# Optimization experiments

Measured on AMD Instinct MI355X. Metric: run time of the kernel, lower is better.

## Reference

```python
import jax, jax.numpy as jnp
import numpy as np

B, C, L, D, E, K = 64, 23, 26000, 64, 512, 3  # batch, chromosomes, bins/chr, d_model, eos_dim, num_states
V = C * L


def setup_inputs() -> dict:
    key = jax.random.key(0)
    k0, k1, k2, k3 = jax.random.split(key, 4)
    return {
        "eos_emb": jax.random.normal(k0, (B, C, E), jnp.float32),
        "bin_ids": jnp.arange(C * L, dtype=jnp.int32).reshape(C, L),
        "emb_table": jax.random.normal(k1, (V, D), jnp.float32) * 0.02,
        "eos_W": jax.random.normal(k2, (D, E), jnp.float32) / np.float32(np.sqrt(E)),
        "eos_b": jnp.zeros((D,), jnp.float32),
        "fc_W": jax.random.normal(k3, (K, 2 * D), jnp.float32) / np.float32(np.sqrt(2 * D)),
        "fc_b": jnp.zeros((K,), jnp.float32),
    }


def reference(eos_emb, bin_ids, emb_table, eos_W, eos_b, fc_W, fc_b):
    # eos_projection (use_eos_proj=True): [B,C,E] @ [D,E]^T + b -> [B,C,D]
    eos = jnp.einsum('bce,de->bcd', eos_emb, eos_W) + eos_b
    # per-chromosome embedding gather (bin_projection skipped: bin_emb_dim == d_model, use_bin_proj=False)
    bin_emb = emb_table[bin_ids]  # [C,L,D]
    # fc on concat([bin, eos]) == bin @ Wb^T + eos @ We^T + b (avoids materializing [B,C,L,2D])
    Wb, We = fc_W[:, :D], fc_W[:, D:]
    a = jnp.einsum('cld,kd->clk', bin_emb, Wb)          # [C,L,K]
    e = jnp.einsum('bcd,kd->bck', eos, We) + fc_b       # [B,C,K]
    return jax.nn.relu(a[None, :, :, :] + e[:, :, None, :])  # [B,C,L,K]
```

## Files before the change

kernel.cpp:

```cpp
#include <hip/hip_runtime.h>

#define NB 64
#define NC 23
#define NL 26000
#define ND 64
#define NE 512
#define NK 3
#define NCL (NC * NL)
#define FP4 (NL * NK / 4)
#define BSTRIDE4 ((size_t)NC * FP4)

typedef float v4f __attribute__((ext_vector_type(4)));

__global__ __launch_bounds__(64) void eos_e_kernel(
    const float* __restrict__ eos_emb,
    const float* __restrict__ eos_W,
    const float* __restrict__ eos_b,
    const float* __restrict__ fc_W,
    const float* __restrict__ fc_b,
    float* __restrict__ e_out)
{
    const int bc = blockIdx.x;
    const int d  = threadIdx.x;

    __shared__ float xs[NE];
    float4* xs4 = reinterpret_cast<float4*>(xs);
    const float4* src = reinterpret_cast<const float4*>(eos_emb + (size_t)bc * NE);
    for (int i = d; i < NE / 4; i += 64) xs4[i] = src[i];
    __syncthreads();

    const float4* wrow = reinterpret_cast<const float4*>(eos_W + (size_t)d * NE);
    float acc = 0.f;
    #pragma unroll 8
    for (int i = 0; i < NE / 4; ++i) {
        float4 w = wrow[i];
        float4 x = xs4[i];
        acc += w.x * x.x;
        acc += w.y * x.y;
        acc += w.z * x.z;
        acc += w.w * x.w;
    }
    const float eosd = acc + eos_b[d];

    #pragma unroll
    for (int k = 0; k < NK; ++k) {
        float p = eosd * fc_W[k * (2 * ND) + ND + d];
        #pragma unroll
        for (int off = 32; off > 0; off >>= 1) p += __shfl_xor(p, off, 64);
        if (d == 0) e_out[(size_t)bc * NK + k] = p + fc_b[k];
    }
}

__global__ __launch_bounds__(256) void a_kernel(
    const int*   __restrict__ bin_ids,
    const float* __restrict__ emb_table,
    const float* __restrict__ fc_W,
    float* __restrict__ a_out)
{
    const int c   = blockIdx.y;
    const int tid = threadIdx.x;
    const int l   = blockIdx.x * 256 + tid;

    __shared__ float wb[NK][ND];
    if (tid < NK * ND)
        wb[tid / ND][tid % ND] = fc_W[(tid / ND) * (2 * ND) + (tid % ND)];
    __syncthreads();
    if (l >= NL) return;

    const int row = bin_ids[(size_t)c * NL + l];
    const float4* er = reinterpret_cast<const float4*>(emb_table + (size_t)row * ND);
    const float4* w0 = reinterpret_cast<const float4*>(wb[0]);
    const float4* w1 = reinterpret_cast<const float4*>(wb[1]);
    const float4* w2 = reinterpret_cast<const float4*>(wb[2]);

    float a0 = 0.f, a1 = 0.f, a2 = 0.f;
    #pragma unroll
    for (int i = 0; i < ND / 4; ++i) {
        float4 v  = er[i];
        float4 p0 = w0[i], p1 = w1[i], p2 = w2[i];
        a0 += v.x * p0.x + v.y * p0.y + v.z * p0.z + v.w * p0.w;
        a1 += v.x * p1.x + v.y * p1.y + v.z * p1.z + v.w * p1.w;
        a2 += v.x * p2.x + v.y * p2.y + v.z * p2.z + v.w * p2.w;
    }

    float* dst = a_out + ((size_t)c * NL + l) * NK;
    dst[0] = a0; dst[1] = a1; dst[2] = a2;
}

__global__ __launch_bounds__(256) void bstream_kernel(
    const float* __restrict__ a_in,
    const float* __restrict__ e_in,
    float* __restrict__ out)
{
    const int c  = blockIdx.y;
    const int bx = blockIdx.x;
    const int t  = threadIdx.x;

    __shared__ v4f e4[3][66];
    if (t < 3 * NB) {
        const int p = t >> 6;
        const int b = t & 63;
        const float* ep = e_in + ((size_t)b * NC + c) * NK;
        const float e0 = ep[0], e1 = ep[1], e2 = ep[2];
        v4f v;
        if      (p == 0) { v.x = e0; v.y = e1; v.z = e2; v.w = e0; }
        else if (p == 1) { v.x = e1; v.y = e2; v.z = e0; v.w = e1; }
        else             { v.x = e2; v.y = e0; v.z = e1; v.w = e2; }
        e4[p][b] = v;
    }
    __syncthreads();

    const int f0 = bx * 768 + t;
    const int f1 = f0 + 256;
    const int f2 = f0 + 512;
    const bool g0 = f0 < FP4, g1 = f1 < FP4, g2 = f2 < FP4;

    const v4f* a4 = reinterpret_cast<const v4f*>(a_in) + (size_t)c * FP4;
    v4f av0 = (v4f)(0.f), av1 = (v4f)(0.f), av2 = (v4f)(0.f);
    if (g0) av0 = __builtin_nontemporal_load(&a4[f0]);
    if (g1) av1 = __builtin_nontemporal_load(&a4[f1]);
    if (g2) av2 = __builtin_nontemporal_load(&a4[f2]);

    const v4f* ep0 = &e4[f0 % 3][0];
    const v4f* ep1 = &e4[f1 % 3][0];
    const v4f* ep2 = &e4[f2 % 3][0];

    v4f* o4 = reinterpret_cast<v4f*>(out);
    size_t i0 = (size_t)c * FP4 + f0;
    size_t i1 = (size_t)c * FP4 + f1;
    size_t i2 = (size_t)c * FP4 + f2;

    #pragma unroll 4
    for (int b = 0; b < NB; ++b) {
        if (g0) {
            const v4f ev = ep0[b];
            v4f o;
            o.x = fmaxf(av0.x + ev.x, 0.f);
            o.y = fmaxf(av0.y + ev.y, 0.f);
            o.z = fmaxf(av0.z + ev.z, 0.f);
            o.w = fmaxf(av0.w + ev.w, 0.f);
            __builtin_nontemporal_store(o, &o4[i0]);
        }
        if (g1) {
            const v4f ev = ep1[b];
            v4f o;
            o.x = fmaxf(av1.x + ev.x, 0.f);
            o.y = fmaxf(av1.y + ev.y, 0.f);
            o.z = fmaxf(av1.z + ev.z, 0.f);
            o.w = fmaxf(av1.w + ev.w, 0.f);
            __builtin_nontemporal_store(o, &o4[i1]);
        }
        if (g2) {
            const v4f ev = ep2[b];
            v4f o;
            o.x = fmaxf(av2.x + ev.x, 0.f);
            o.y = fmaxf(av2.y + ev.y, 0.f);
            o.z = fmaxf(av2.z + ev.z, 0.f);
            o.w = fmaxf(av2.w + ev.w, 0.f);
            __builtin_nontemporal_store(o, &o4[i2]);
        }
        i0 += BSTRIDE4;
        i1 += BSTRIDE4;
        i2 += BSTRIDE4;
    }
}

__global__ __launch_bounds__(256) void decoder_fused_kernel(
    const int*   __restrict__ bin_ids,
    const float* __restrict__ emb_table,
    const float* __restrict__ fc_W,
    const float* __restrict__ e_in,
    float* __restrict__ out)
{
    const int c   = blockIdx.y;
    const int tid = threadIdx.x;
    const int l   = blockIdx.x * 256 + tid;

    __shared__ float wb[NK][ND];
    __shared__ float es[NB * NK];

    if (tid < NK * ND)
        wb[tid / ND][tid % ND] = fc_W[(tid / ND) * (2 * ND) + (tid % ND)];
    if (tid < NB * NK) {
        int b = tid / NK, k = tid % NK;
        es[tid] = e_in[((size_t)b * NC + c) * NK + k];
    }
    __syncthreads();
    if (l >= NL) return;

    const int row = bin_ids[(size_t)c * NL + l];
    const float4* er = reinterpret_cast<const float4*>(emb_table + (size_t)row * ND);
    const float4* w0 = reinterpret_cast<const float4*>(wb[0]);
    const float4* w1 = reinterpret_cast<const float4*>(wb[1]);
    const float4* w2 = reinterpret_cast<const float4*>(wb[2]);

    float a0 = 0.f, a1 = 0.f, a2 = 0.f;
    #pragma unroll
    for (int i = 0; i < ND / 4; ++i) {
        float4 v  = er[i];
        float4 p0 = w0[i], p1 = w1[i], p2 = w2[i];
        a0 += v.x * p0.x + v.y * p0.y + v.z * p0.z + v.w * p0.w;
        a1 += v.x * p1.x + v.y * p1.y + v.z * p1.z + v.w * p1.w;
        a2 += v.x * p2.x + v.y * p2.y + v.z * p2.z + v.w * p2.w;
    }

    size_t obase = ((size_t)c * NL + l) * NK;
    const size_t bstride = (size_t)NC * NL * NK;
    #pragma unroll 4
    for (int b = 0; b < NB; ++b) {
        const float e0 = es[b * NK + 0];
        const float e1 = es[b * NK + 1];
        const float e2 = es[b * NK + 2];
        out[obase + 0] = fmaxf(a0 + e0, 0.f);
        out[obase + 1] = fmaxf(a1 + e1, 0.f);
        out[obase + 2] = fmaxf(a2 + e2, 0.f);
        obase += bstride;
    }
}

extern "C" void kernel_launch(void* const* d_in, const int* in_sizes, int n_in,
                              void* d_out, int out_size, void* d_ws, size_t ws_size,
                              hipStream_t stream) {
    const float* eos_emb   = (const float*)d_in[0];
    const int*   bin_ids   = (const int*)  d_in[1];
    const float* emb_table = (const float*)d_in[2];
    const float* eos_W     = (const float*)d_in[3];
    const float* eos_b     = (const float*)d_in[4];
    const float* fc_W      = (const float*)d_in[5];
    const float* fc_b      = (const float*)d_in[6];
    float*       out       = (float*)d_out;

    float*  e_ws = (float*)d_ws;
    const size_t a_off_bytes = 32768;
    float*  a_ws = (float*)((char*)d_ws + a_off_bytes);
    const size_t a_bytes = (size_t)NC * NL * NK * sizeof(float);

    eos_e_kernel<<<NB * NC, 64, 0, stream>>>(eos_emb, eos_W, eos_b, fc_W, fc_b, e_ws);

    if (ws_size >= a_off_bytes + a_bytes) {
        dim3 grid_a((NL + 255) / 256, NC);
        a_kernel<<<grid_a, 256, 0, stream>>>(bin_ids, emb_table, fc_W, a_ws);

        dim3 grid_b((FP4 + 767) / 768, NC);
        bstream_kernel<<<grid_b, 256, 0, stream>>>(a_ws, e_ws, out);
    } else {
        dim3 grid((NL + 255) / 256, NC);
        decoder_fused_kernel<<<grid, 256, 0, stream>>>(bin_ids, emb_table, fc_W, e_ws, out);
    }
}
```

Baseline: 162.0 us.

## Split reductions across lane quads and batch-split the broadcast stream kernel

The eos projection now gives each output dimension to four lanes that reduce with shuffles, so each block runs 256 threads instead of 64. The bin projection kernel likewise uses four lanes per bin, which coalesces its embedding-row reads. The bstream kernel adds a grid z-dimension that splits the batch into four chunks of 16 for more parallelism, at the cost of re-reading the intermediate a array four times. Nontemporal loads and stores are replaced with ordinary ones, which changes how the large output write interacts with the cache.

Result: faster. 147.9 us (-8.7%).

```diff
diff --git a/kernel.cpp b/kernel.cpp
--- a/kernel.cpp
+++ b/kernel.cpp
@@ -12,7 +12,7 @@
 
 typedef float v4f __attribute__((ext_vector_type(4)));
 
-__global__ __launch_bounds__(64) void eos_e_kernel(
+__global__ __launch_bounds__(256) void eos_e_kernel(
     const float* __restrict__ eos_emb,
     const float* __restrict__ eos_W,
     const float* __restrict__ eos_b,
@@ -21,34 +21,41 @@
     float* __restrict__ e_out)
 {
     const int bc = blockIdx.x;
-    const int d  = threadIdx.x;
-
-    __shared__ float xs[NE];
-    float4* xs4 = reinterpret_cast<float4*>(xs);
-    const float4* src = reinterpret_cast<const float4*>(eos_emb + (size_t)bc * NE);
-    for (int i = d; i < NE / 4; i += 64) xs4[i] = src[i];
-    __syncthreads();
-
-    const float4* wrow = reinterpret_cast<const float4*>(eos_W + (size_t)d * NE);
-    float acc = 0.f;
+    const int t  = threadIdx.x;
+    const int q  = t & 3;
+    const int d  = t >> 2;
+
+    __shared__ v4f xs4[NE / 4];
+    if (t < NE / 4)
+        xs4[t] = reinterpret_cast<const v4f*>(eos_emb + (size_t)bc * NE)[t];
+    __syncthreads();
+
+    const v4f* wrow = reinterpret_cast<const v4f*>(eos_W + (size_t)d * NE);
+    v4f acc = (v4f)(0.f);
     #pragma unroll 8
-    for (int i = 0; i < NE / 4; ++i) {
-        float4 w = wrow[i];
-        float4 x = xs4[i];
-        acc += w.x * x.x;
-        acc += w.y * x.y;
-        acc += w.z * x.z;
-        acc += w.w * x.w;
-    }
-    const float eosd = acc + eos_b[d];
-
+    for (int j = 0; j < NE / 16; ++j) {
+        const int idx = q + 4 * j;
+        acc += wrow[idx] * xs4[idx];
+    }
+    float p = (acc.x + acc.y) + (acc.z + acc.w);
+    p += __shfl_xor(p, 1, 64);
+    p += __shfl_xor(p, 2, 64);
+    const float eosd = p + eos_b[d];
+
+    __shared__ float part[4][NK];
     #pragma unroll
     for (int k = 0; k < NK; ++k) {
-        float p = eosd * fc_W[k * (2 * ND) + ND + d];
-        #pragma unroll
-        for (int off = 32; off > 0; off >>= 1) p += __shfl_xor(p, off, 64);
-        if (d == 0) e_out[(size_t)bc * NK + k] = p + fc_b[k];
-    }
+        float pk = eosd * fc_W[k * (2 * ND) + ND + d];
+        pk += __shfl_xor(pk,  4, 64);
+        pk += __shfl_xor(pk,  8, 64);
+        pk += __shfl_xor(pk, 16, 64);
+        pk += __shfl_xor(pk, 32, 64);
+        if ((t & 63) == 0) part[t >> 6][k] = pk;
+    }
+    __syncthreads();
+    if (t < NK)
+        e_out[(size_t)bc * NK + t] =
+            part[0][t] + part[1][t] + part[2][t] + part[3][t] + fc_b[t];
 }
 
 __global__ __launch_bounds__(256) void a_kernel(
@@ -57,34 +64,43 @@
     const float* __restrict__ fc_W,
     float* __restrict__ a_out)
 {
-    const int c   = blockIdx.y;
-    const int tid = threadIdx.x;
-    const int l   = blockIdx.x * 256 + tid;
-
-    __shared__ float wb[NK][ND];
-    if (tid < NK * ND)
-        wb[tid / ND][tid % ND] = fc_W[(tid / ND) * (2 * ND) + (tid % ND)];
+    const int c = blockIdx.y;
+    const int t = threadIdx.x;
+    const int q = t & 3;
+    const int r = t >> 2;
+    const int l = blockIdx.x * 64 + r;
+
+    __shared__ v4f wb4[NK][ND / 4];
+    if (t < NK * (ND / 4)) {
+        const int k = t / (ND / 4), i = t % (ND / 4);
+        wb4[k][i] = reinterpret_cast<const v4f*>(fc_W + (size_t)k * (2 * ND))[i];
+    }
     __syncthreads();
     if (l >= NL) return;
 
     const int row = bin_ids[(size_t)c * NL + l];
-    const float4* er = reinterpret_cast<const float4*>(emb_table + (size_t)row * ND);
-    const float4* w0 = reinterpret_cast<const float4*>(wb[0]);
-    const float4* w1 = reinterpret_cast<const float4*>(wb[1]);
-    const float4* w2 = reinterpret_cast<const float4*>(wb[2]);
-
-    float a0 = 0.f, a1 = 0.f, a2 = 0.f;
+    const v4f* er = reinterpret_cast<const v4f*>(emb_table + (size_t)row * ND);
+
+    v4f s0 = (v4f)(0.f), s1 = (v4f)(0.f), s2 = (v4f)(0.f);
     #pragma unroll
-    for (int i = 0; i < ND / 4; ++i) {
-        float4 v  = er[i];
-        float4 p0 = w0[i], p1 = w1[i], p2 = w2[i];
-        a0 += v.x * p0.x + v.y * p0.y + v.z * p0.z + v.w * p0.w;
-        a1 += v.x * p1.x + v.y * p1.y + v.z * p1.z + v.w * p1.w;
-        a2 += v.x * p2.x + v.y * p2.y + v.z * p2.z + v.w * p2.w;
-    }
-
-    float* dst = a_out + ((size_t)c * NL + l) * NK;
-    dst[0] = a0; dst[1] = a1; dst[2] = a2;
+    for (int j = 0; j < 4; ++j) {
+        const int idx = q + 4 * j;
+        const v4f v = er[idx];
+        s0 += v * wb4[0][idx];
+        s1 += v * wb4[1][idx];
+        s2 += v * wb4[2][idx];
+    }
+    float a0 = (s0.x + s0.y) + (s0.z + s0.w);
+    float a1 = (s1.x + s1.y) + (s1.z + s1.w);
+    float a2 = (s2.x + s2.y) + (s2.z + s2.w);
+    a0 += __shfl_xor(a0, 1, 64); a0 += __shfl_xor(a0, 2, 64);
+    a1 += __shfl_xor(a1, 1, 64); a1 += __shfl_xor(a1, 2, 64);
+    a2 += __shfl_xor(a2, 1, 64); a2 += __shfl_xor(a2, 2, 64);
+
+    if (q < NK) {
+        const float val = (q == 0) ? a0 : (q == 1) ? a1 : a2;
+        a_out[((size_t)c * NL + l) * NK + q] = val;
+    }
 }
 
 __global__ __launch_bounds__(256) void bstream_kernel(
@@ -92,21 +108,22 @@
     const float* __restrict__ e_in,
     float* __restrict__ out)
 {
+    const int bx = blockIdx.x;
     const int c  = blockIdx.y;
-    const int bx = blockIdx.x;
+    const int b0 = blockIdx.z * 16;
     const int t  = threadIdx.x;
 
-    __shared__ v4f e4[3][66];
-    if (t < 3 * NB) {
-        const int p = t >> 6;
-        const int b = t & 63;
-        const float* ep = e_in + ((size_t)b * NC + c) * NK;
+    __shared__ v4f e4[3][17];
+    if (t < 3 * 16) {
+        const int p  = t >> 4;
+        const int bl = t & 15;
+        const float* ep = e_in + ((size_t)(b0 + bl) * NC + c) * NK;
         const float e0 = ep[0], e1 = ep[1], e2 = ep[2];
         v4f v;
         if      (p == 0) { v.x = e0; v.y = e1; v.z = e2; v.w = e0; }
         else if (p == 1) { v.x = e1; v.y = e2; v.z = e0; v.w = e1; }
         else             { v.x = e2; v.y = e0; v.z = e1; v.w = e2; }
-        e4[p][b] = v;
+        e4[p][bl] = v;
     }
     __syncthreads();
 
@@ -117,47 +134,47 @@
 
     const v4f* a4 = reinterpret_cast<const v4f*>(a_in) + (size_t)c * FP4;
     v4f av0 = (v4f)(0.f), av1 = (v4f)(0.f), av2 = (v4f)(0.f);
-    if (g0) av0 = __builtin_nontemporal_load(&a4[f0]);
-    if (g1) av1 = __builtin_nontemporal_load(&a4[f1]);
-    if (g2) av2 = __builtin_nontemporal_load(&a4[f2]);
+    if (g0) av0 = a4[f0];
+    if (g1) av1 = a4[f1];
+    if (g2) av2 = a4[f2];
 
     const v4f* ep0 = &e4[f0 % 3][0];
     const v4f* ep1 = &e4[f1 % 3][0];
     const v4f* ep2 = &e4[f2 % 3][0];
 
     v4f* o4 = reinterpret_cast<v4f*>(out);
-    size_t i0 = (size_t)c * FP4 + f0;
-    size_t i1 = (size_t)c * FP4 + f1;
-    size_t i2 = (size_t)c * FP4 + f2;
+    size_t i0 = (size_t)b0 * BSTRIDE4 + (size_t)c * FP4 + f0;
+    size_t i1 = i0 + 256;
+    size_t i2 = i0 + 512;
 
     #pragma unroll 4
-    for (int b = 0; b < NB; ++b) {
+    for (int bl = 0; bl < 16; ++bl) {
         if (g0) {
-            const v4f ev = ep0[b];
+            const v4f ev = ep0[bl];
             v4f o;
             o.x = fmaxf(av0.x + ev.x, 0.f);
             o.y = fmaxf(av0.y + ev.y, 0.f);
             o.z = fmaxf(av0.z + ev.z, 0.f);
             o.w = fmaxf(av0.w + ev.w, 0.f);
-            __builtin_nontemporal_store(o, &o4[i0]);
+            o4[i0] = o;
         }
         if (g1) {
-            const v4f ev = ep1[b];
+            const v4f ev = ep1[bl];
             v4f o;
             o.x = fmaxf(av1.x + ev.x, 0.f);
             o.y = fmaxf(av1.y + ev.y, 0.f);
             o.z = fmaxf(av1.z + ev.z, 0.f);
             o.w = fmaxf(av1.w + ev.w, 0.f);
-            __builtin_nontemporal_store(o, &o4[i1]);
+            o4[i1] = o;
         }
         if (g2) {
-            const v4f ev = ep2[b];
+            const v4f ev = ep2[bl];
             v4f o;
             o.x = fmaxf(av2.x + ev.x, 0.f);
             o.y = fmaxf(av2.y + ev.y, 0.f);
             o.z = fmaxf(av2.z + ev.z, 0.f);
             o.w = fmaxf(av2.w + ev.w, 0.f);
-            __builtin_nontemporal_store(o, &o4[i2]);
+            o4[i2] = o;
         }
         i0 += BSTRIDE4;
         i1 += BSTRIDE4;
@@ -235,13 +252,13 @@
     float*  a_ws = (float*)((char*)d_ws + a_off_bytes);
     const size_t a_bytes = (size_t)NC * NL * NK * sizeof(float);
 
-    eos_e_kernel<<<NB * NC, 64, 0, stream>>>(eos_emb, eos_W, eos_b, fc_W, fc_b, e_ws);
+    eos_e_kernel<<<NB * NC, 256, 0, stream>>>(eos_emb, eos_W, eos_b, fc_W, fc_b, e_ws);
 
     if (ws_size >= a_off_bytes + a_bytes) {
-        dim3 grid_a((NL + 255) / 256, NC);
+        dim3 grid_a((NL + 63) / 64, NC);
         a_kernel<<<grid_a, 256, 0, stream>>>(bin_ids, emb_table, fc_W, a_ws);
 
-        dim3 grid_b((FP4 + 767) / 768, NC);
+        dim3 grid_b((FP4 + 767) / 768, NC, 4);
         bstream_kernel<<<grid_b, 256, 0, stream>>>(a_ws, e_ws, out);
     } else {
         dim3 grid((NL + 255) / 256, NC);
```
